# Performance work log

Measured on AMD Instinct MI355X. Metric: run time of the kernel, lower is better.

The kernel has to match this reference:

```python
import jax, jax.numpy as jnp
import numpy as np

N_EMBD = 1024
N_HEAD = 16
HEAD_SIZE = N_EMBD // N_HEAD  # 64

def setup_inputs() -> dict:
    key = jax.random.key(0)
    ks = jax.random.split(key, 6)
    B, T, C, H, S = 2, 2048, N_EMBD, N_HEAD, HEAD_SIZE
    sc = 1.0 / np.sqrt(C)
    x = jax.random.normal(ks[0], (B, T, C), dtype=jnp.float32)
    # stacked per-head projection weights (no bias), [H, C, S]
    Wq = jax.random.normal(ks[1], (H, C, S), dtype=jnp.float32) * sc
    Wk = jax.random.normal(ks[2], (H, C, S), dtype=jnp.float32) * sc
    Wv = jax.random.normal(ks[3], (H, C, S), dtype=jnp.float32) * sc
    Wp = jax.random.normal(ks[4], (C, C), dtype=jnp.float32) * sc
    bp = jax.random.normal(ks[5], (C,), dtype=jnp.float32) * 0.01
    return {"x": x, "Wq": Wq, "Wk": Wk, "Wv": Wv, "Wp": Wp, "bp": bp}

def reference(x, Wq, Wk, Wv, Wp, bp):
    # Eval-mode forward (dropout = identity), default non-flash path.
    B, T, C = x.shape
    H, _, S = Wq.shape
    q = jnp.einsum('btc,hcs->bhts', x, Wq)
    k = jnp.einsum('btc,hcs->bhts', x, Wk)
    v = jnp.einsum('btc,hcs->bhts', x, Wv)
    att = jnp.einsum('bhts,bhus->bhtu', q, k) * (1.0 / np.sqrt(S))
    causal = jnp.tril(jnp.ones((T, T), dtype=bool))
    att = jnp.where(causal[None, None], att, -jnp.inf)
    att = jax.nn.softmax(att, axis=-1)
    y = jnp.einsum('bhtu,bhus->bhts', att, v)
    # concat heads along feature dim (head-major), then output projection
    y = y.transpose(0, 2, 1, 3).reshape(B, T, H * S)
    return y @ Wp.T + bp
```

## Files before the change

### kernel.cpp

```cpp
#include <hip/hip_runtime.h>
#include <hip/hip_bf16.h>
#include <cmath>

typedef __attribute__((ext_vector_type(8))) short bf16x8;
typedef __attribute__((ext_vector_type(4))) float f32x4;
typedef __attribute__((ext_vector_type(16))) float f32x16;

__device__ __forceinline__ unsigned short f2bf(float f) {
    union { float f; unsigned int i; } c; c.f = f;
    unsigned int i = c.i;
    unsigned int r = i + 0x7FFF + ((i >> 16) & 1);
    return (unsigned short)(r >> 16);
}

__device__ __forceinline__ float fast_exp2(float x) {
    float r;
    asm("v_exp_f32 %0, %1" : "=v"(r) : "v"(x));
    return r;
}

__device__ __forceinline__ void gload_lds16(const unsigned short* g, unsigned short* l) {
    __builtin_amdgcn_global_load_lds((const __attribute__((address_space(1))) unsigned int*)g,
                                     (__attribute__((address_space(3))) unsigned int*)l, 16, 0, 0);
}

__global__ void k_cvt(const float* __restrict__ src, unsigned short* __restrict__ dst, int n4) {
    int i = blockIdx.x * blockDim.x + threadIdx.x;
    if (i < n4) {
        float4 v = reinterpret_cast<const float4*>(src)[i];
        ushort4 o;
        o.x = f2bf(v.x); o.y = f2bf(v.y); o.z = f2bf(v.z); o.w = f2bf(v.w);
        reinterpret_cast<ushort4*>(dst)[i] = o;
    }
}

__global__ void k_cvt_wt(const float* __restrict__ Wq, const float* __restrict__ Wk,
                         const float* __restrict__ Wv, unsigned short* __restrict__ Wt) {
    __shared__ unsigned short lt[64][72];
    int bid = blockIdx.x;
    int ct  = bid & 15;
    int h   = (bid >> 4) & 15;
    int sec = bid >> 8;
    const float* W = (sec == 0) ? Wq : ((sec == 1) ? Wk : Wv);
    float sc = (sec == 0) ? 0.1803368801f : 1.0f;
    int t = threadIdx.x;
    #pragma unroll
    for (int q = 0; q < 4; q++) {
        int id = t + q * 256;
        int c  = id >> 4;
        int s4 = (id & 15) * 4;
        float4 v = *reinterpret_cast<const float4*>(&W[((size_t)(h * 1024) + (ct * 64 + c)) * 64 + s4]);
        lt[s4 + 0][c] = f2bf(v.x * sc);
        lt[s4 + 1][c] = f2bf(v.y * sc);
        lt[s4 + 2][c] = f2bf(v.z * sc);
        lt[s4 + 3][c] = f2bf(v.w * sc);
    }
    __syncthreads();
    #pragma unroll
    for (int q = 0; q < 2; q++) {
        int id = t + q * 256;
        int s  = id >> 3;
        int c8 = (id & 7) * 8;
        bf16x8 val = *reinterpret_cast<const bf16x8*>(&lt[s][c8]);
        int n = sec * 1024 + h * 64 + s;
        *reinterpret_cast<bf16x8*>(&Wt[(size_t)n * 1024 + ct * 64 + c8]) = val;
    }
}

template <int MODE>
__launch_bounds__(256, 2)
__global__ void k_gemm(const unsigned short* __restrict__ A,
                       const unsigned short* __restrict__ Bt,
                       int M, int N, int K,
                       unsigned short* __restrict__ q_nat,
                       unsigned short* __restrict__ k_nat,
                       unsigned short* __restrict__ vT,
                       float* __restrict__ out, const float* __restrict__ bp) {
    __shared__ unsigned short Asm[2][128][64];
    __shared__ unsigned short Bsm[2][128][64];
    const int nb = N >> 7;
    int cpx = gridDim.x >> 3;
    int bid = (blockIdx.x & 7) * cpx + (blockIdx.x >> 3);
    int n0 = (bid % nb) << 7;
    int m0 = (bid / nb) << 7;
    int t = threadIdx.x;
    int lane = t & 63, w = t >> 6;
    int wr = w >> 1, wc = w & 1;
    int l15 = lane & 15, lg = lane >> 4;
    int sr = lane >> 3;
    int scol = ((lane & 7) ^ sr) << 3;

    f32x4 acc[4][4];
    #pragma unroll
    for (int i = 0; i < 4; i++)
        #pragma unroll
        for (int j = 0; j < 4; j++) acc[i][j] = (f32x4){0.f, 0.f, 0.f, 0.f};

    auto STAGE = [&](int kt, int buf) {
        #pragma unroll
        for (int q = 0; q < 4; q++) {
            int rb = q * 32 + w * 8;
            int row = rb + sr;
            gload_lds16(&A[(size_t)(m0 + row) * K + kt + scol], &Asm[buf][rb][0]);
            gload_lds16(&Bt[(size_t)(n0 + row) * K + kt + scol], &Bsm[buf][rb][0]);
        }
    };

    const int NT = K >> 6;
    STAGE(0, 0);
    asm volatile("s_waitcnt vmcnt(0)" ::: "memory");
    __builtin_amdgcn_s_barrier();
    int cur = 0;

    for (int tt = 0; tt < NT; tt++) {
        if (tt + 1 < NT) STAGE((tt + 1) << 6, cur ^ 1);

        bf16x8 af[4][2], bfr[4][2];
        int x15 = (l15 & 7) << 3;
        #pragma unroll
        for (int mi = 0; mi < 4; mi++) {
            int row = wr * 64 + mi * 16 + l15;
            af[mi][0] = *reinterpret_cast<const bf16x8*>(&Asm[cur][row][(lg * 8) ^ x15]);
            af[mi][1] = *reinterpret_cast<const bf16x8*>(&Asm[cur][row][(32 + lg * 8) ^ x15]);
        }
        #pragma unroll
        for (int nj = 0; nj < 4; nj++) {
            int row = wc * 64 + nj * 16 + l15;
            bfr[nj][0] = *reinterpret_cast<const bf16x8*>(&Bsm[cur][row][(lg * 8) ^ x15]);
            bfr[nj][1] = *reinterpret_cast<const bf16x8*>(&Bsm[cur][row][(32 + lg * 8) ^ x15]);
        }
        asm volatile("s_waitcnt lgkmcnt(0)" ::: "memory");
        __builtin_amdgcn_sched_barrier(0);
        __builtin_amdgcn_s_setprio(1);
        #pragma unroll
        for (int mi = 0; mi < 4; mi++)
            #pragma unroll
            for (int nj = 0; nj < 4; nj++) {
                acc[mi][nj] = __builtin_amdgcn_mfma_f32_16x16x32_bf16(af[mi][0], bfr[nj][0], acc[mi][nj], 0, 0, 0);
                acc[mi][nj] = __builtin_amdgcn_mfma_f32_16x16x32_bf16(af[mi][1], bfr[nj][1], acc[mi][nj], 0, 0, 0);
            }
        __builtin_amdgcn_s_setprio(0);

        asm volatile("s_waitcnt vmcnt(0)" ::: "memory");
        __builtin_amdgcn_s_barrier();
        cur ^= 1;
    }

    unsigned short* qkdst = nullptr;
    int noff = 0;
    if (MODE == 0) { qkdst = (n0 < 1024) ? q_nat : k_nat; noff = (n0 < 1024) ? 0 : 1024; }
    #pragma unroll
    for (int mi = 0; mi < 4; mi++) {
        #pragma unroll
        for (int nj = 0; nj < 4; nj++) {
            #pragma unroll
            for (int r = 0; r < 4; r++) {
                int m = m0 + wr * 64 + mi * 16 + lg * 4 + r;
                int n = n0 + wc * 64 + nj * 16 + l15;
                float v = acc[mi][nj][r];
                if (MODE == 0) {
                    qkdst[(size_t)m * 1024 + (n - noff)] = f2bf(v);
                } else if (MODE == 2) {
                    int bb = n >> 11, ttn = n & 2047;
                    int hh = m >> 6, ss = m & 63;
                    vT[(((size_t)(bb * 16 + hh)) * 64 + ss) * 2048 + ttn] = f2bf(v);
                } else {
                    out[(size_t)m * 1024 + n] = v + bp[n];
                }
            }
        }
    }
}

__launch_bounds__(256, 4)
__global__ void k_attn(const unsigned short* __restrict__ q_nat,
                       const unsigned short* __restrict__ k_nat,
                       const unsigned short* __restrict__ vT,
                       unsigned short* __restrict__ y_bf) {
    __shared__ __align__(16) unsigned short Ks[2][64][64];
    __shared__ __align__(16) unsigned short Vs[2][64][64];
    __shared__ float clB[64];
    const int T = 2048, H = 16;
    int bid = blockIdx.x;
    int bh = bid & 31;
    int qi = 31 - (bid >> 5);
    int h = bh & 15, b = bh >> 4;
    int t = threadIdx.x;
    int lane = t & 63, w = t >> 6;
    int pr = w >> 1, rg = w & 1;
    int l31 = lane & 31, hi = lane >> 5;
    int warp_q0 = qi * 64 + rg * 32;
    int qg = warp_q0 + l31;

    int n0 = (qi >> 1) + 1;
    int nS = pr ? ((qi + 1) >> 1) : n0;

    const unsigned short* kbase = k_nat + (size_t)(b * T) * 1024 + h * 64;
    const unsigned short* vbase = vT + ((size_t)(b * H + h) * 64) * 2048;

    int sxor = ((lane & 7) ^ (lane >> 3)) << 3;

    auto STAGE = [&](int j) {
        #pragma unroll
        for (int r = 0; r < 4; r++) {
            int rb = r * 16 + rg * 8;
            int grow = rb + (lane >> 3);
            gload_lds16(kbase + (size_t)(j * 64 + grow) * 1024 + sxor, &Ks[pr][rb][0]);
            gload_lds16(vbase + (size_t)grow * 2048 + j * 64 + sxor, &Vs[pr][rb][0]);
        }
    };

    bf16x8 qf[4];
    #pragma unroll
    for (int tt = 0; tt < 4; tt++)
        qf[tt] = *reinterpret_cast<const bf16x8*>(
            q_nat + (size_t)(b * T + qg) * 1024 + h * 64 + tt * 16 + hi * 8);

    bf16x8 ones;
    #pragma unroll
    for (int z = 0; z < 8; z++) ones[z] = (short)0x3F80;

    f32x16 acc0, acc1, lacc;
    #pragma unroll
    for (int r = 0; r < 16; r++) { acc0[r] = 0.f; acc1[r] = 0.f; lacc[r] = 0.f; }

    for (int i = 0; i < n0; i++) {
        bool act = (i < nS);
        int j = pr + 2 * i;
        if (act) STAGE(j);
        __syncthreads();

        if (act) {
            const char* kb = (const char*)&Ks[pr][0][0];
            const char* vb = (const char*)&Vs[pr][0][0];
            int rsw = (l31 & 7) << 4;

            f32x16 s0, s1;
            #pragma unroll
            for (int r = 0; r < 16; r++) { s0[r] = 0.f; s1[r] = 0.f; }
            __builtin_amdgcn_s_setprio(1);
            #pragma unroll
            for (int tt = 0; tt < 4; tt++) {
                int cb = (tt * 32 + hi * 16) ^ rsw;
                bf16x8 kf0 = *reinterpret_cast<const bf16x8*>(kb + l31 * 128 + cb);
                bf16x8 kf1 = *reinterpret_cast<const bf16x8*>(kb + (32 + l31) * 128 + cb);
                s0 = __builtin_amdgcn_mfma_f32_32x32x16_bf16(kf0, qf[tt], s0, 0, 0, 0);
                s1 = __builtin_amdgcn_mfma_f32_32x32x16_bf16(kf1, qf[tt], s1, 0, 0, 0);
            }
            __builtin_amdgcn_s_setprio(0);

            if (j == qi) {
                #pragma unroll
                for (int r = 0; r < 16; r++) {
                    int kvr = (r & 3) + 8 * (r >> 2) + 4 * hi + j * 64;
                    if (kvr > qg) s0[r] = -INFINITY;
                    if (kvr + 32 > qg) s1[r] = -INFINITY;
                }
            }

            #pragma unroll
            for (int r = 0; r < 16; r++) {
                s0[r] = fast_exp2(s0[r]);
                s1[r] = fast_exp2(s1[r]);
            }

            unsigned int c[16];
            #pragma unroll
            for (int i2 = 0; i2 < 8; i2++) {
                asm("v_cvt_pk_bf16_f32 %0, %1, %2" : "=v"(c[i2]) : "v"(s0[2 * i2]), "v"(s0[2 * i2 + 1]));
                asm("v_cvt_pk_bf16_f32 %0, %1, %2" : "=v"(c[8 + i2]) : "v"(s1[2 * i2]), "v"(s1[2 * i2 + 1]));
            }
            bf16x8 pa[4];
            #pragma unroll
            for (int ks = 0; ks < 4; ks++) {
                unsigned int clo0 = c[ks * 4 + 0], clo1 = c[ks * 4 + 1];
                unsigned int chi0 = c[ks * 4 + 2], chi1 = c[ks * 4 + 3];
                unsigned int pl0 = (unsigned int)__shfl_xor((int)clo0, 32, 64);
                unsigned int pl1 = (unsigned int)__shfl_xor((int)clo1, 32, 64);
                unsigned int ph0 = (unsigned int)__shfl_xor((int)chi0, 32, 64);
                unsigned int ph1 = (unsigned int)__shfl_xor((int)chi1, 32, 64);
                union { unsigned int u[4]; bf16x8 v; } fr;
                fr.u[0] = hi ? ph0 : clo0;
                fr.u[1] = hi ? ph1 : clo1;
                fr.u[2] = hi ? chi0 : pl0;
                fr.u[3] = hi ? chi1 : pl1;
                pa[ks] = fr.v;
            }

            __builtin_amdgcn_s_setprio(1);
            #pragma unroll
            for (int ks = 0; ks < 4; ks++) {
                int cb = (ks * 32 + hi * 16) ^ rsw;
                bf16x8 v0 = *reinterpret_cast<const bf16x8*>(vb + l31 * 128 + cb);
                bf16x8 v1 = *reinterpret_cast<const bf16x8*>(vb + (32 + l31) * 128 + cb);
                acc0 = __builtin_amdgcn_mfma_f32_32x32x16_bf16(pa[ks], v0, acc0, 0, 0, 0);
                acc1 = __builtin_amdgcn_mfma_f32_32x32x16_bf16(pa[ks], v1, acc1, 0, 0, 0);
                lacc = __builtin_amdgcn_mfma_f32_32x32x16_bf16(pa[ks], ones, lacc, 0, 0, 0);
            }
            __builtin_amdgcn_s_setprio(0);
        }

        __syncthreads();
    }

    float* Ocomb = (float*)&Ks[0][0][0];
    if (pr == 1) {
        #pragma unroll
        for (int r = 0; r < 16; r++) {
            int qr = (r & 3) + 8 * (r >> 2) + 4 * hi;
            Ocomb[(rg * 32 + qr) * 64 + l31] = acc0[r];
            Ocomb[(rg * 32 + qr) * 64 + 32 + l31] = acc1[r];
            if (l31 == 0) clB[rg * 32 + qr] = lacc[r];
        }
    }
    __syncthreads();
    if (pr == 0) {
        #pragma unroll
        for (int r = 0; r < 16; r++) {
            int qr = (r & 3) + 8 * (r >> 2) + 4 * hi;
            float lt = lacc[r] + clB[rg * 32 + qr];
            float dv = 1.0f / lt;
            float o0 = acc0[r] + Ocomb[(rg * 32 + qr) * 64 + l31];
            float o1 = acc1[r] + Ocomb[(rg * 32 + qr) * 64 + 32 + l31];
            size_t row = (size_t)(b * T + warp_q0 + qr) * 1024 + h * 64;
            y_bf[row + l31] = f2bf(o0 * dv);
            y_bf[row + 32 + l31] = f2bf(o1 * dv);
        }
    }
}

extern "C" void kernel_launch(void* const* d_in, const int* in_sizes, int n_in,
                              void* d_out, int out_size, void* d_ws, size_t ws_size,
                              hipStream_t stream) {
    const float* x  = (const float*)d_in[0];
    const float* Wq = (const float*)d_in[1];
    const float* Wk = (const float*)d_in[2];
    const float* Wv = (const float*)d_in[3];
    const float* Wp = (const float*)d_in[4];
    const float* bp = (const float*)d_in[5];
    float* out = (float*)d_out;

    char* ws = (char*)d_ws;
    unsigned short* x_bf  = (unsigned short*)(ws);
    unsigned short* Wt    = (unsigned short*)(ws + ((size_t)8  << 20));
    unsigned short* Wp_bf = (unsigned short*)(ws + ((size_t)14 << 20));
    unsigned short* q_nat = (unsigned short*)(ws + ((size_t)16 << 20));
    unsigned short* k_nat = (unsigned short*)(ws + ((size_t)24 << 20));
    unsigned short* vT    = (unsigned short*)(ws + ((size_t)32 << 20));
    unsigned short* y_bf  = (unsigned short*)(ws + ((size_t)40 << 20));

    k_cvt<<<4096, 256, 0, stream>>>(x, x_bf, 4194304 / 4);
    k_cvt<<<1024, 256, 0, stream>>>(Wp, Wp_bf, 1048576 / 4);
    k_cvt_wt<<<768, 256, 0, stream>>>(Wq, Wk, Wv, Wt);
    k_gemm<0><<<32 * 16, 256, 0, stream>>>(x_bf, Wt, 4096, 2048, 1024,
                                           q_nat, k_nat, nullptr, nullptr, nullptr);
    k_gemm<2><<<8 * 32, 256, 0, stream>>>(Wt + (size_t)2048 * 1024, x_bf, 1024, 4096, 1024,
                                          nullptr, nullptr, vT, nullptr, nullptr);
    k_attn<<<1024, 256, 0, stream>>>(q_nat, k_nat, vT, y_bf);
    k_gemm<1><<<32 * 8, 256, 0, stream>>>(y_bf, Wp_bf, 4096, 1024, 1024,
                                          nullptr, nullptr, nullptr, out, bp);
}
```

Baseline: 121.9 us.

## Retile attention to 128-query blocks and merge conversion and QKV launches

Attention now uses 512-thread blocks that each cover 128 queries, so every K/V tile staged in LDS feeds four query warps instead of two. Both key-split halves now run the same number of iterations, which removes the idle-iteration predication. The three fp32-to-bf16 conversion kernels are merged into one launch, and the Q/K and V projection GEMMs are merged into one 768-block launch, cutting launch count and tail gaps. The cost is more masked work on the diagonal tiles and fewer, larger attention blocks, which can lower occupancy flexibility.

```diff
diff --git a/kernel.cpp b/kernel.cpp
--- a/kernel.cpp
+++ b/kernel.cpp
@@ -24,26 +24,30 @@
                                      (__attribute__((address_space(3))) unsigned int*)l, 16, 0, 0);
 }
 
-__global__ void k_cvt(const float* __restrict__ src, unsigned short* __restrict__ dst, int n4) {
-    int i = blockIdx.x * blockDim.x + threadIdx.x;
-    if (i < n4) {
+__global__ void k_cvt_all(const float* __restrict__ x, const float* __restrict__ Wp,
+                          const float* __restrict__ Wq, const float* __restrict__ Wk,
+                          const float* __restrict__ Wv,
+                          unsigned short* __restrict__ x_bf, unsigned short* __restrict__ Wp_bf,
+                          unsigned short* __restrict__ Wt) {
+    __shared__ unsigned short lt[64][72];
+    int bid = blockIdx.x;
+    int t = threadIdx.x;
+    if (bid < 5120) {
+        const float* src = (bid < 4096) ? x : Wp;
+        unsigned short* dst = (bid < 4096) ? x_bf : Wp_bf;
+        int i = ((bid < 4096) ? bid : (bid - 4096)) * 256 + t;
         float4 v = reinterpret_cast<const float4*>(src)[i];
         ushort4 o;
         o.x = f2bf(v.x); o.y = f2bf(v.y); o.z = f2bf(v.z); o.w = f2bf(v.w);
         reinterpret_cast<ushort4*>(dst)[i] = o;
-    }
-}
-
-__global__ void k_cvt_wt(const float* __restrict__ Wq, const float* __restrict__ Wk,
-                         const float* __restrict__ Wv, unsigned short* __restrict__ Wt) {
-    __shared__ unsigned short lt[64][72];
-    int bid = blockIdx.x;
-    int ct  = bid & 15;
-    int h   = (bid >> 4) & 15;
-    int sec = bid >> 8;
+        return;
+    }
+    int sub = bid - 5120;
+    int ct  = sub & 15;
+    int h   = (sub >> 4) & 15;
+    int sec = sub >> 8;
     const float* W = (sec == 0) ? Wq : ((sec == 1) ? Wk : Wv);
     float sc = (sec == 0) ? 0.1803368801f : 1.0f;
-    int t = threadIdx.x;
     #pragma unroll
     for (int q = 0; q < 4; q++) {
         int id = t + q * 256;
@@ -67,18 +71,280 @@
     }
 }
 
-template <int MODE>
 __launch_bounds__(256, 2)
-__global__ void k_gemm(const unsigned short* __restrict__ A,
-                       const unsigned short* __restrict__ Bt,
-                       int M, int N, int K,
-                       unsigned short* __restrict__ q_nat,
-                       unsigned short* __restrict__ k_nat,
-                       unsigned short* __restrict__ vT,
-                       float* __restrict__ out, const float* __restrict__ bp) {
+__global__ void k_gemm_qkv(const unsigned short* __restrict__ x_bf,
+                           const unsigned short* __restrict__ Wt,
+                           unsigned short* __restrict__ q_nat,
+                           unsigned short* __restrict__ k_nat,
+                           unsigned short* __restrict__ vT) {
     __shared__ unsigned short Asm[2][128][64];
     __shared__ unsigned short Bsm[2][128][64];
-    const int nb = N >> 7;
+    const int K = 1024;
+    int cpx = gridDim.x >> 3;
+    int bid = (blockIdx.x & 7) * cpx + (blockIdx.x >> 3);
+    bool isV = (bid >= 512);
+    const unsigned short* A;
+    const unsigned short* Bt;
+    int m0, n0;
+    if (!isV) {
+        n0 = (bid & 15) << 7;
+        m0 = (bid >> 4) << 7;
+        A = x_bf; Bt = Wt;
+    } else {
+        int vb = bid - 512;
+        n0 = (vb & 31) << 7;
+        m0 = (vb >> 5) << 7;
+        A = Wt + (size_t)2048 * 1024;
+        Bt = x_bf;
+    }
+    int t = threadIdx.x;
+    int lane = t & 63, w = t >> 6;
+    int wr = w >> 1, wc = w & 1;
+    int l15 = lane & 15, lg = lane >> 4;
+    int sr = lane >> 3;
+    int scol = ((lane & 7) ^ sr) << 3;
+
+    f32x4 acc[4][4];
+    #pragma unroll
+    for (int i = 0; i < 4; i++)
+        #pragma unroll
+        for (int j = 0; j < 4; j++) acc[i][j] = (f32x4){0.f, 0.f, 0.f, 0.f};
+
+    auto STAGE = [&](int kt, int buf) {
+        #pragma unroll
+        for (int q = 0; q < 4; q++) {
+            int rb = q * 32 + w * 8;
+            int row = rb + sr;
+            gload_lds16(&A[(size_t)(m0 + row) * K + kt + scol], &Asm[buf][rb][0]);
+            gload_lds16(&Bt[(size_t)(n0 + row) * K + kt + scol], &Bsm[buf][rb][0]);
+        }
+    };
+
+    const int NT = K >> 6;
+    STAGE(0, 0);
+    asm volatile("s_waitcnt vmcnt(0)" ::: "memory");
+    __builtin_amdgcn_s_barrier();
+    int cur = 0;
+
+    for (int tt = 0; tt < NT; tt++) {
+        if (tt + 1 < NT) STAGE((tt + 1) << 6, cur ^ 1);
+
+        bf16x8 af[4][2], bfr[4][2];
+        int x15 = (l15 & 7) << 3;
+        #pragma unroll
+        for (int mi = 0; mi < 4; mi++) {
+            int row = wr * 64 + mi * 16 + l15;
+            af[mi][0] = *reinterpret_cast<const bf16x8*>(&Asm[cur][row][(lg * 8) ^ x15]);
+            af[mi][1] = *reinterpret_cast<const bf16x8*>(&Asm[cur][row][(32 + lg * 8) ^ x15]);
+        }
+        #pragma unroll
+        for (int nj = 0; nj < 4; nj++) {
+            int row = wc * 64 + nj * 16 + l15;
+            bfr[nj][0] = *reinterpret_cast<const bf16x8*>(&Bsm[cur][row][(lg * 8) ^ x15]);
+            bfr[nj][1] = *reinterpret_cast<const bf16x8*>(&Bsm[cur][row][(32 + lg * 8) ^ x15]);
+        }
+        asm volatile("s_waitcnt lgkmcnt(0)" ::: "memory");
+        __builtin_amdgcn_sched_barrier(0);
+        __builtin_amdgcn_s_setprio(1);
+        #pragma unroll
+        for (int mi = 0; mi < 4; mi++)
+            #pragma unroll
+            for (int nj = 0; nj < 4; nj++) {
+                acc[mi][nj] = __builtin_amdgcn_mfma_f32_16x16x32_bf16(af[mi][0], bfr[nj][0], acc[mi][nj], 0, 0, 0);
+                acc[mi][nj] = __builtin_amdgcn_mfma_f32_16x16x32_bf16(af[mi][1], bfr[nj][1], acc[mi][nj], 0, 0, 0);
+            }
+        __builtin_amdgcn_s_setprio(0);
+
+        asm volatile("s_waitcnt vmcnt(0)" ::: "memory");
+        __builtin_amdgcn_s_barrier();
+        cur ^= 1;
+    }
+
+    unsigned short* qkdst = nullptr;
+    int noff = 0;
+    if (!isV) { qkdst = (n0 < 1024) ? q_nat : k_nat; noff = (n0 < 1024) ? 0 : 1024; }
+    #pragma unroll
+    for (int mi = 0; mi < 4; mi++) {
+        #pragma unroll
+        for (int nj = 0; nj < 4; nj++) {
+            #pragma unroll
+            for (int r = 0; r < 4; r++) {
+                int m = m0 + wr * 64 + mi * 16 + lg * 4 + r;
+                int n = n0 + wc * 64 + nj * 16 + l15;
+                float v = acc[mi][nj][r];
+                if (!isV) {
+                    qkdst[(size_t)m * 1024 + (n - noff)] = f2bf(v);
+                } else {
+                    int bb = n >> 11, ttn = n & 2047;
+                    int hh = m >> 6, ss = m & 63;
+                    vT[(((size_t)(bb * 16 + hh)) * 64 + ss) * 2048 + ttn] = f2bf(v);
+                }
+            }
+        }
+    }
+}
+
+__launch_bounds__(512, 4)
+__global__ void k_attn(const unsigned short* __restrict__ q_nat,
+                       const unsigned short* __restrict__ k_nat,
+                       const unsigned short* __restrict__ vT,
+                       unsigned short* __restrict__ y_bf) {
+    __shared__ __align__(16) unsigned short SM[2][2][64][64];
+    __shared__ float clB[128];
+    const int T = 2048, H = 16;
+    int bid = blockIdx.x;
+    int bh = bid & 31;
+    int p  = 15 - (bid >> 5);
+    int h = bh & 15, b = bh >> 4;
+    int t = threadIdx.x;
+    int lane = t & 63, w = t >> 6;
+    int pr = w >> 2, rg = w & 3;
+    int l31 = lane & 31, hi = lane >> 5;
+    int q0 = p << 7;
+    int warp_q0 = q0 + rg * 32;
+    int qg = warp_q0 + l31;
+    int nS = p + 1;
+
+    const unsigned short* kbase = k_nat + (size_t)(b * T) * 1024 + h * 64;
+    const unsigned short* vbase = vT + ((size_t)(b * H + h) * 64) * 2048;
+
+    int sxor = ((lane & 7) ^ (lane >> 3)) << 3;
+
+    auto STAGE = [&](int j) {
+        #pragma unroll
+        for (int r = 0; r < 2; r++) {
+            int rb = r * 32 + rg * 8;
+            int grow = rb + (lane >> 3);
+            gload_lds16(kbase + (size_t)(j * 64 + grow) * 1024 + sxor, &SM[0][pr][rb][0]);
+            gload_lds16(vbase + (size_t)grow * 2048 + j * 64 + sxor, &SM[1][pr][rb][0]);
+        }
+    };
+
+    bf16x8 qf[4];
+    #pragma unroll
+    for (int tt = 0; tt < 4; tt++)
+        qf[tt] = *reinterpret_cast<const bf16x8*>(
+            q_nat + (size_t)(b * T + qg) * 1024 + h * 64 + tt * 16 + hi * 8);
+
+    bf16x8 ones;
+    #pragma unroll
+    for (int z = 0; z < 8; z++) ones[z] = (short)0x3F80;
+
+    f32x16 acc0, acc1, lacc;
+    #pragma unroll
+    for (int r = 0; r < 16; r++) { acc0[r] = 0.f; acc1[r] = 0.f; lacc[r] = 0.f; }
+
+    for (int i = 0; i < nS; i++) {
+        int j = pr + 2 * i;
+        STAGE(j);
+        __syncthreads();
+
+        const char* kb = (const char*)&SM[0][pr][0][0];
+        const char* vb = (const char*)&SM[1][pr][0][0];
+        int rsw = (l31 & 7) << 4;
+
+        f32x16 s0, s1;
+        #pragma unroll
+        for (int r = 0; r < 16; r++) { s0[r] = 0.f; s1[r] = 0.f; }
+        __builtin_amdgcn_s_setprio(1);
+        #pragma unroll
+        for (int tt = 0; tt < 4; tt++) {
+            int cb = (tt * 32 + hi * 16) ^ rsw;
+            bf16x8 kf0 = *reinterpret_cast<const bf16x8*>(kb + l31 * 128 + cb);
+            bf16x8 kf1 = *reinterpret_cast<const bf16x8*>(kb + (32 + l31) * 128 + cb);
+            s0 = __builtin_amdgcn_mfma_f32_32x32x16_bf16(kf0, qf[tt], s0, 0, 0, 0);
+            s1 = __builtin_amdgcn_mfma_f32_32x32x16_bf16(kf1, qf[tt], s1, 0, 0, 0);
+        }
+        __builtin_amdgcn_s_setprio(0);
+
+        if (j * 64 + 63 > warp_q0) {
+            #pragma unroll
+            for (int r = 0; r < 16; r++) {
+                int kvr = (r & 3) + 8 * (r >> 2) + 4 * hi + j * 64;
+                if (kvr > qg) s0[r] = -INFINITY;
+                if (kvr + 32 > qg) s1[r] = -INFINITY;
+            }
+        }
+
+        #pragma unroll
+        for (int r = 0; r < 16; r++) {
+            s0[r] = fast_exp2(s0[r]);
+            s1[r] = fast_exp2(s1[r]);
+        }
+
+        unsigned int c[16];
+        #pragma unroll
+        for (int i2 = 0; i2 < 8; i2++) {
+            asm("v_cvt_pk_bf16_f32 %0, %1, %2" : "=v"(c[i2]) : "v"(s0[2 * i2]), "v"(s0[2 * i2 + 1]));
+            asm("v_cvt_pk_bf16_f32 %0, %1, %2" : "=v"(c[8 + i2]) : "v"(s1[2 * i2]), "v"(s1[2 * i2 + 1]));
+        }
+        bf16x8 pa[4];
+        #pragma unroll
+        for (int ks = 0; ks < 4; ks++) {
+            unsigned int clo0 = c[ks * 4 + 0], clo1 = c[ks * 4 + 1];
+            unsigned int chi0 = c[ks * 4 + 2], chi1 = c[ks * 4 + 3];
+            unsigned int pl0 = (unsigned int)__shfl_xor((int)clo0, 32, 64);
+            unsigned int pl1 = (unsigned int)__shfl_xor((int)clo1, 32, 64);
+            unsigned int ph0 = (unsigned int)__shfl_xor((int)chi0, 32, 64);
+            unsigned int ph1 = (unsigned int)__shfl_xor((int)chi1, 32, 64);
+            union { unsigned int u[4]; bf16x8 v; } fr;
+            fr.u[0] = hi ? ph0 : clo0;
+            fr.u[1] = hi ? ph1 : clo1;
+            fr.u[2] = hi ? chi0 : pl0;
+            fr.u[3] = hi ? chi1 : pl1;
+            pa[ks] = fr.v;
+        }
+
+        __builtin_amdgcn_s_setprio(1);
+        #pragma unroll
+        for (int ks = 0; ks < 4; ks++) {
+            int cb = (ks * 32 + hi * 16) ^ rsw;
+            bf16x8 v0 = *reinterpret_cast<const bf16x8*>(vb + l31 * 128 + cb);
+            bf16x8 v1 = *reinterpret_cast<const bf16x8*>(vb + (32 + l31) * 128 + cb);
+            acc0 = __builtin_amdgcn_mfma_f32_32x32x16_bf16(pa[ks], v0, acc0, 0, 0, 0);
+            acc1 = __builtin_amdgcn_mfma_f32_32x32x16_bf16(pa[ks], v1, acc1, 0, 0, 0);
+            lacc = __builtin_amdgcn_mfma_f32_32x32x16_bf16(pa[ks], ones, lacc, 0, 0, 0);
+        }
+        __builtin_amdgcn_s_setprio(0);
+
+        __syncthreads();
+    }
+
+    float* Ocomb = (float*)&SM[0][0][0][0];
+    if (pr == 1) {
+        #pragma unroll
+        for (int r = 0; r < 16; r++) {
+            int qr = (r & 3) + 8 * (r >> 2) + 4 * hi;
+            int rr = rg * 32 + qr;
+            Ocomb[rr * 64 + l31] = acc0[r];
+            Ocomb[rr * 64 + 32 + l31] = acc1[r];
+            if (l31 == 0) clB[rr] = lacc[r];
+        }
+    }
+    __syncthreads();
+    if (pr == 0) {
+        #pragma unroll
+        for (int r = 0; r < 16; r++) {
+            int qr = (r & 3) + 8 * (r >> 2) + 4 * hi;
+            int rr = rg * 32 + qr;
+            float lt2 = lacc[r] + clB[rr];
+            float dv = 1.0f / lt2;
+            float o0 = acc0[r] + Ocomb[rr * 64 + l31];
+            float o1 = acc1[r] + Ocomb[rr * 64 + 32 + l31];
+            size_t row = (size_t)(b * T + q0 + rr) * 1024 + h * 64;
+            y_bf[row + l31] = f2bf(o0 * dv);
+            y_bf[row + 32 + l31] = f2bf(o1 * dv);
+        }
+    }
+}
+
+__launch_bounds__(256, 2)
+__global__ void k_gemm_proj(const unsigned short* __restrict__ A,
+                            const unsigned short* __restrict__ Bt,
+                            float* __restrict__ out, const float* __restrict__ bp) {
+    __shared__ unsigned short Asm[2][128][64];
+    __shared__ unsigned short Bsm[2][128][64];
+    const int K = 1024, nb = 8;
     int cpx = gridDim.x >> 3;
     int bid = (blockIdx.x & 7) * cpx + (blockIdx.x >> 3);
     int n0 = (bid % nb) << 7;
@@ -114,7 +380,6 @@
 
     for (int tt = 0; tt < NT; tt++) {
         if (tt + 1 < NT) STAGE((tt + 1) << 6, cur ^ 1);
-
         bf16x8 af[4][2], bfr[4][2];
         int x15 = (l15 & 7) << 3;
         #pragma unroll
@@ -140,193 +405,21 @@
                 acc[mi][nj] = __builtin_amdgcn_mfma_f32_16x16x32_bf16(af[mi][1], bfr[nj][1], acc[mi][nj], 0, 0, 0);
             }
         __builtin_amdgcn_s_setprio(0);
-
         asm volatile("s_waitcnt vmcnt(0)" ::: "memory");
         __builtin_amdgcn_s_barrier();
         cur ^= 1;
     }
 
-    unsigned short* qkdst = nullptr;
-    int noff = 0;
-    if (MODE == 0) { qkdst = (n0 < 1024) ? q_nat : k_nat; noff = (n0 < 1024) ? 0 : 1024; }
-    #pragma unroll
-    for (int mi = 0; mi < 4; mi++) {
-        #pragma unroll
-        for (int nj = 0; nj < 4; nj++) {
+    #pragma unroll
+    for (int mi = 0; mi < 4; mi++)
+        #pragma unroll
+        for (int nj = 0; nj < 4; nj++)
             #pragma unroll
             for (int r = 0; r < 4; r++) {
                 int m = m0 + wr * 64 + mi * 16 + lg * 4 + r;
                 int n = n0 + wc * 64 + nj * 16 + l15;
-                float v = acc[mi][nj][r];
-                if (MODE == 0) {
-                    qkdst[(size_t)m * 1024 + (n - noff)] = f2bf(v);
-                } else if (MODE == 2) {
-                    int bb = n >> 11, ttn = n & 2047;
-                    int hh = m >> 6, ss = m & 63;
-                    vT[(((size_t)(bb * 16 + hh)) * 64 + ss) * 2048 + ttn] = f2bf(v);
-                } else {
-                    out[(size_t)m * 1024 + n] = v + bp[n];
-                }
+                out[(size_t)m * 1024 + n] = acc[mi][nj][r] + bp[n];
             }
-        }
-    }
-}
-
-__launch_bounds__(256, 4)
-__global__ void k_attn(const unsigned short* __restrict__ q_nat,
-                       const unsigned short* __restrict__ k_nat,
-                       const unsigned short* __restrict__ vT,
-                       unsigned short* __restrict__ y_bf) {
-    __shared__ __align__(16) unsigned short Ks[2][64][64];
-    __shared__ __align__(16) unsigned short Vs[2][64][64];
-    __shared__ float clB[64];
-    const int T = 2048, H = 16;
-    int bid = blockIdx.x;
-    int bh = bid & 31;
-    int qi = 31 - (bid >> 5);
-    int h = bh & 15, b = bh >> 4;
-    int t = threadIdx.x;
-    int lane = t & 63, w = t >> 6;
-    int pr = w >> 1, rg = w & 1;
-    int l31 = lane & 31, hi = lane >> 5;
-    int warp_q0 = qi * 64 + rg * 32;
-    int qg = warp_q0 + l31;
-
-    int n0 = (qi >> 1) + 1;
-    int nS = pr ? ((qi + 1) >> 1) : n0;
-
-    const unsigned short* kbase = k_nat + (size_t)(b * T) * 1024 + h * 64;
-    const unsigned short* vbase = vT + ((size_t)(b * H + h) * 64) * 2048;
-
-    int sxor = ((lane & 7) ^ (lane >> 3)) << 3;
-
-    auto STAGE = [&](int j) {
-        #pragma unroll
-        for (int r = 0; r < 4; r++) {
-            int rb = r * 16 + rg * 8;
-            int grow = rb + (lane >> 3);
-            gload_lds16(kbase + (size_t)(j * 64 + grow) * 1024 + sxor, &Ks[pr][rb][0]);
-            gload_lds16(vbase + (size_t)grow * 2048 + j * 64 + sxor, &Vs[pr][rb][0]);
-        }
-    };
-
-    bf16x8 qf[4];
-    #pragma unroll
-    for (int tt = 0; tt < 4; tt++)
-        qf[tt] = *reinterpret_cast<const bf16x8*>(
-            q_nat + (size_t)(b * T + qg) * 1024 + h * 64 + tt * 16 + hi * 8);
-
-    bf16x8 ones;
-    #pragma unroll
-    for (int z = 0; z < 8; z++) ones[z] = (short)0x3F80;
-
-    f32x16 acc0, acc1, lacc;
-    #pragma unroll
-    for (int r = 0; r < 16; r++) { acc0[r] = 0.f; acc1[r] = 0.f; lacc[r] = 0.f; }
-
-    for (int i = 0; i < n0; i++) {
-        bool act = (i < nS);
-        int j = pr + 2 * i;
-        if (act) STAGE(j);
-        __syncthreads();
-
-        if (act) {
-            const char* kb = (const char*)&Ks[pr][0][0];
-            const char* vb = (const char*)&Vs[pr][0][0];
-            int rsw = (l31 & 7) << 4;
-
-            f32x16 s0, s1;
-            #pragma unroll
-            for (int r = 0; r < 16; r++) { s0[r] = 0.f; s1[r] = 0.f; }
-            __builtin_amdgcn_s_setprio(1);
-            #pragma unroll
-            for (int tt = 0; tt < 4; tt++) {
-                int cb = (tt * 32 + hi * 16) ^ rsw;
-                bf16x8 kf0 = *reinterpret_cast<const bf16x8*>(kb + l31 * 128 + cb);
-                bf16x8 kf1 = *reinterpret_cast<const bf16x8*>(kb + (32 + l31) * 128 + cb);
-                s0 = __builtin_amdgcn_mfma_f32_32x32x16_bf16(kf0, qf[tt], s0, 0, 0, 0);
-                s1 = __builtin_amdgcn_mfma_f32_32x32x16_bf16(kf1, qf[tt], s1, 0, 0, 0);
-            }
-            __builtin_amdgcn_s_setprio(0);
-
-            if (j == qi) {
-                #pragma unroll
-                for (int r = 0; r < 16; r++) {
-                    int kvr = (r & 3) + 8 * (r >> 2) + 4 * hi + j * 64;
-                    if (kvr > qg) s0[r] = -INFINITY;
-                    if (kvr + 32 > qg) s1[r] = -INFINITY;
-                }
-            }
-
-            #pragma unroll
-            for (int r = 0; r < 16; r++) {
-                s0[r] = fast_exp2(s0[r]);
-                s1[r] = fast_exp2(s1[r]);
-            }
-
-            unsigned int c[16];
-            #pragma unroll
-            for (int i2 = 0; i2 < 8; i2++) {
-                asm("v_cvt_pk_bf16_f32 %0, %1, %2" : "=v"(c[i2]) : "v"(s0[2 * i2]), "v"(s0[2 * i2 + 1]));
-                asm("v_cvt_pk_bf16_f32 %0, %1, %2" : "=v"(c[8 + i2]) : "v"(s1[2 * i2]), "v"(s1[2 * i2 + 1]));
-            }
-            bf16x8 pa[4];
-            #pragma unroll
-            for (int ks = 0; ks < 4; ks++) {
-                unsigned int clo0 = c[ks * 4 + 0], clo1 = c[ks * 4 + 1];
-                unsigned int chi0 = c[ks * 4 + 2], chi1 = c[ks * 4 + 3];
-                unsigned int pl0 = (unsigned int)__shfl_xor((int)clo0, 32, 64);
-                unsigned int pl1 = (unsigned int)__shfl_xor((int)clo1, 32, 64);
-                unsigned int ph0 = (unsigned int)__shfl_xor((int)chi0, 32, 64);
-                unsigned int ph1 = (unsigned int)__shfl_xor((int)chi1, 32, 64);
-                union { unsigned int u[4]; bf16x8 v; } fr;
-                fr.u[0] = hi ? ph0 : clo0;
-                fr.u[1] = hi ? ph1 : clo1;
-                fr.u[2] = hi ? chi0 : pl0;
-                fr.u[3] = hi ? chi1 : pl1;
-                pa[ks] = fr.v;
-            }
-
-            __builtin_amdgcn_s_setprio(1);
-            #pragma unroll
-            for (int ks = 0; ks < 4; ks++) {
-                int cb = (ks * 32 + hi * 16) ^ rsw;
-                bf16x8 v0 = *reinterpret_cast<const bf16x8*>(vb + l31 * 128 + cb);
-                bf16x8 v1 = *reinterpret_cast<const bf16x8*>(vb + (32 + l31) * 128 + cb);
-                acc0 = __builtin_amdgcn_mfma_f32_32x32x16_bf16(pa[ks], v0, acc0, 0, 0, 0);
-                acc1 = __builtin_amdgcn_mfma_f32_32x32x16_bf16(pa[ks], v1, acc1, 0, 0, 0);
-                lacc = __builtin_amdgcn_mfma_f32_32x32x16_bf16(pa[ks], ones, lacc, 0, 0, 0);
-            }
-            __builtin_amdgcn_s_setprio(0);
-        }
-
-        __syncthreads();
-    }
-
-    float* Ocomb = (float*)&Ks[0][0][0];
-    if (pr == 1) {
-        #pragma unroll
-        for (int r = 0; r < 16; r++) {
-            int qr = (r & 3) + 8 * (r >> 2) + 4 * hi;
-            Ocomb[(rg * 32 + qr) * 64 + l31] = acc0[r];
-            Ocomb[(rg * 32 + qr) * 64 + 32 + l31] = acc1[r];
-            if (l31 == 0) clB[rg * 32 + qr] = lacc[r];
-        }
-    }
-    __syncthreads();
-    if (pr == 0) {
-        #pragma unroll
-        for (int r = 0; r < 16; r++) {
-            int qr = (r & 3) + 8 * (r >> 2) + 4 * hi;
-            float lt = lacc[r] + clB[rg * 32 + qr];
-            float dv = 1.0f / lt;
-            float o0 = acc0[r] + Ocomb[(rg * 32 + qr) * 64 + l31];
-            float o1 = acc1[r] + Ocomb[(rg * 32 + qr) * 64 + 32 + l31];
-            size_t row = (size_t)(b * T + warp_q0 + qr) * 1024 + h * 64;
-            y_bf[row + l31] = f2bf(o0 * dv);
-            y_bf[row + 32 + l31] = f2bf(o1 * dv);
-        }
-    }
 }
 
 extern "C" void kernel_launch(void* const* d_in, const int* in_sizes, int n_in,
@@ -349,14 +442,8 @@
     unsigned short* vT    = (unsigned short*)(ws + ((size_t)32 << 20));
     unsigned short* y_bf  = (unsigned short*)(ws + ((size_t)40 << 20));
 
-    k_cvt<<<4096, 256, 0, stream>>>(x, x_bf, 4194304 / 4);
-    k_cvt<<<1024, 256, 0, stream>>>(Wp, Wp_bf, 1048576 / 4);
-    k_cvt_wt<<<768, 256, 0, stream>>>(Wq, Wk, Wv, Wt);
-    k_gemm<0><<<32 * 16, 256, 0, stream>>>(x_bf, Wt, 4096, 2048, 1024,
-                                           q_nat, k_nat, nullptr, nullptr, nullptr);
-    k_gemm<2><<<8 * 32, 256, 0, stream>>>(Wt + (size_t)2048 * 1024, x_bf, 1024, 4096, 1024,
-                                          nullptr, nullptr, vT, nullptr, nullptr);
-    k_attn<<<1024, 256, 0, stream>>>(q_nat, k_nat, vT, y_bf);
-    k_gemm<1><<<32 * 8, 256, 0, stream>>>(y_bf, Wp_bf, 4096, 1024, 1024,
-                                          nullptr, nullptr, nullptr, out, bp);
-}
+    k_cvt_all<<<5888, 256, 0, stream>>>(x, Wp, Wq, Wk, Wv, x_bf, Wp_bf, Wt);
+    k_gemm_qkv<<<768, 256, 0, stream>>>(x_bf, Wt, q_nat, k_nat, vT);
+    k_attn<<<512, 512, 0, stream>>>(q_nat, k_nat, vT, y_bf);
+    k_gemm_proj<<<256, 256, 0, stream>>>(y_bf, Wp_bf, out, bp);
+}
```

Result: faster. 111.1 us (-8.9%).
